# Performance work log

Hardware: AMD Instinct MI355X
Metric: run time of the kernel (lower is better)

## Reference

```python
import jax, jax.numpy as jnp
import numpy as np
from functools import partial

N_NODES = 50000
BN_EPS = 1e-5


def _renumber(src, dst, mask, n_nodes):
    # Faithful to extract_batch_edge_idx: kept edges are relabeled by the rank of
    # their node id among the sorted unique node ids APPEARING in kept edges.
    m = mask.astype(jnp.int32)
    appear = jnp.zeros(n_nodes, jnp.int32)
    appear = appear.at[src].max(m)
    appear = appear.at[dst].max(m)
    new_id = jnp.cumsum(appear) - 1  # rank of each appearing node id
    s = jnp.where(mask, new_id[src], 0)
    d = jnp.where(mask, new_id[dst], 0)
    return s, d


def _gcn_conv(x, W, b, src, dst, ew, n):
    # PyG GCNConv: linear, add self-loops, symmetric normalization, scatter-add.
    xw = x @ W                                   # [n, out]
    deg = jax.ops.segment_sum(ew, dst, num_segments=n) + 1.0  # +1 self loop
    dinv = jax.lax.rsqrt(deg)
    norm = dinv[src] * dinv[dst] * ew            # masked edges -> 0 weight
    agg = jax.ops.segment_sum(norm[:, None] * xw[src], dst, num_segments=n)
    agg = agg + (dinv * dinv)[:, None] * xw      # self-loop contribution
    return agg + b


def setup_inputs() -> dict:
    key = jax.random.key(0)
    ks = jax.random.split(key, 8)
    R, N, E, B = 3, N_NODES, 1000000, 2048
    inp, hid, out = 256, 512, 256
    features = jax.random.normal(ks[0], (R, N, inp), jnp.float32)
    W1 = jax.random.normal(ks[1], (inp, hid), jnp.float32) * (1.0 / np.sqrt(inp))
    b1 = jnp.zeros((hid,), jnp.float32)
    W2 = jax.random.normal(ks[2], (hid, out), jnp.float32) * (1.0 / np.sqrt(hid))
    b2 = jnp.zeros((out,), jnp.float32)
    gamma = jnp.ones((hid,), jnp.float32)
    beta = jnp.zeros((hid,), jnp.float32)
    edge_index = jax.random.randint(ks[3], (R, 2, E), 0, N, jnp.int64)
    # distinct, sorted batch node ids (torch code iterates node values)
    batch_nodes = jnp.sort(jax.random.permutation(ks[4], N)[:B]).astype(jnp.int64)
    return {"features": features, "W1": W1, "b1": b1, "W2": W2, "b2": b2,
            "gamma": gamma, "beta": beta, "edge_index": edge_index,
            "batch_nodes": batch_nodes}


def reference(features, W1, b1, W2, b2, gamma, beta, edge_index, batch_nodes):
    R, N, _ = features.shape
    B = batch_nodes.shape[0]
    in_batch = jnp.zeros(N, bool).at[batch_nodes].set(True)
    outs = []
    for r in range(R):  # small fixed relation count
        src, dst = edge_index[r, 0], edge_index[r, 1]
        mask = in_batch[src] & in_batch[dst]
        ew = mask.astype(features.dtype)
        s, d = _renumber(src, dst, mask, N)
        x = features[r, batch_nodes]             # [B, inp]
        h = _gcn_conv(x, W1, b1, s, d, ew, B)    # [B, hid]
        # BatchNorm1d (training mode: biased batch stats)
        mu = h.mean(axis=0)
        var = h.var(axis=0)
        h = (h - mu) * jax.lax.rsqrt(var + BN_EPS) * gamma + beta
        outs.append(_gcn_conv(h, W2, b2, s, d, ew, B))  # [B, out]
    stacked = jnp.stack(outs, axis=0)            # [R, B, out]
    return stacked.reshape(B, -1)                # row-major reshape, as torch
```

## Files before the change

### kernel.cpp

```cpp
#include <hip/hip_runtime.h>
#include <hip/hip_bf16.h>
#include <stdint.h>
#include <stddef.h>

#define RNUM   3
#define NNODES 50000
#define ENUM   1000000
#define BATCH  2048
#define INP    256
#define HID    512
#define OUTC   256
#define BN_EPS 1e-5f

typedef __bf16 bf16x8 __attribute__((ext_vector_type(8)));
typedef float  f32x4  __attribute__((ext_vector_type(4)));

__device__ inline unsigned short f2bf(float f) {
    union { float f; unsigned u; } c; c.f = f;
    unsigned u = c.u;
    return (unsigned short)((u + 0x7fffu + ((u >> 16) & 1u)) >> 16);
}

__device__ inline uint4 pack8(float4 a, float4 b) {
    uint4 r;
    r.x = (unsigned)f2bf(a.x) | ((unsigned)f2bf(a.y) << 16);
    r.y = (unsigned)f2bf(a.z) | ((unsigned)f2bf(a.w) << 16);
    r.z = (unsigned)f2bf(b.x) | ((unsigned)f2bf(b.y) << 16);
    r.w = (unsigned)f2bf(b.z) | ((unsigned)f2bf(b.w) << 16);
    return r;
}

__global__ __launch_bounds__(256) void k_wt(const float* __restrict__ W1,
                                            const float* __restrict__ W2,
                                            unsigned short* __restrict__ W1T,
                                            unsigned short* __restrict__ W2T) {
    __shared__ float T[32][33];
    int z = blockIdx.z;
    const float* W = z ? W2 : W1;
    unsigned short* WT = z ? W2T : W1T;
    int K = z ? HID : INP;
    int N = z ? OUTC : HID;
    int kt = blockIdx.y, nt = blockIdx.x;
    if (kt * 32 >= K || nt * 32 >= N) return;
    int tx = threadIdx.x & 31, ty = threadIdx.x >> 5;
#pragma unroll
    for (int j = 0; j < 4; ++j)
        T[ty + j * 8][tx] = W[(size_t)(kt * 32 + ty + j * 8) * N + nt * 32 + tx];
    __syncthreads();
#pragma unroll
    for (int j = 0; j < 4; ++j)
        WT[(size_t)(nt * 32 + ty + j * 8) * K + kt * 32 + tx] = f2bf(T[tx][ty + j * 8]);
}

__global__ void k_prep(const int* __restrict__ bn, int* __restrict__ inv,
                       int* __restrict__ appear, float* __restrict__ deg,
                       float* __restrict__ musum, float* __restrict__ sqsum,
                       int* __restrict__ kcount) {
    int i = blockIdx.x * blockDim.x + threadIdx.x;
    if (i < NNODES) {
        int lo = 0, hi = BATCH;
        while (lo < hi) { int mid = (lo + hi) >> 1; if (bn[mid] < i) lo = mid + 1; else hi = mid; }
        inv[i] = (lo < BATCH && bn[lo] == i) ? lo : -1;
    }
    if (i < RNUM * BATCH) { appear[i] = 0; deg[i] = 0.0f; }
    if (i < RNUM * HID)   { musum[i] = 0.0f; sqsum[i] = 0.0f; }
    if (i < RNUM)         kcount[i] = 0;
}

__global__ void k_mask(const int* __restrict__ edge_index, const int* __restrict__ inv,
                       int* __restrict__ appear, int2* __restrict__ edges,
                       int* __restrict__ kcount) {
    int z = blockIdx.z;
    const int* src = edge_index + (size_t)z * 2 * ENUM;
    const int* dst = src + ENUM;
    int2* ed = edges + (size_t)z * ENUM;
    int* app = appear + z * BATCH;
    int stride = gridDim.x * blockDim.x;
    for (int e4 = blockIdx.x * blockDim.x + threadIdx.x; e4 < ENUM / 4; e4 += stride) {
        int4 s4 = ((const int4*)src)[e4];
        int4 d4 = ((const int4*)dst)[e4];
        int ss[4] = {s4.x, s4.y, s4.z, s4.w};
        int dd[4] = {d4.x, d4.y, d4.z, d4.w};
#pragma unroll
        for (int i = 0; i < 4; ++i) {
            int ps = inv[ss[i]];
            int pd = inv[dd[i]];
            if (ps >= 0 && pd >= 0) {
                int idx = atomicAdd(kcount + z, 1);
                ed[idx] = make_int2(ps, pd);
                app[ps] = 1;
                app[pd] = 1;
            }
        }
    }
}

__global__ __launch_bounds__(1024) void k_scanDeg(const int* __restrict__ appear,
                                                  int2* __restrict__ edges,
                                                  const int* __restrict__ kcount,
                                                  float* __restrict__ deg) {
    __shared__ int buf[2][BATCH];
    __shared__ float degs[BATCH];
    int z = blockIdx.x;
    const int* ap = appear + z * BATCH;
    int2* ed = edges + (size_t)z * ENUM;
    float* dg = deg + z * BATCH;
    int t = threadIdx.x;
    buf[0][t] = ap[t];
    buf[0][t + 1024] = ap[t + 1024];
    degs[t] = 0.0f; degs[t + 1024] = 0.0f;
    __syncthreads();
    int cur = 0;
    for (int off = 1; off < BATCH; off <<= 1) {
        int nxt = cur ^ 1;
        int i1 = t, i2 = t + 1024;
        buf[nxt][i1] = buf[cur][i1] + (i1 >= off ? buf[cur][i1 - off] : 0);
        buf[nxt][i2] = buf[cur][i2] + (i2 >= off ? buf[cur][i2 - off] : 0);
        __syncthreads();
        cur = nxt;
    }
    int K = kcount[z];
    for (int e = t; e < K; e += 1024) {
        int2 E = ed[e];
        int s = buf[cur][E.x] - 1;
        int d = buf[cur][E.y] - 1;
        ed[e] = make_int2(s, d);
        atomicAdd(&degs[d], 1.0f);
    }
    __syncthreads();
    dg[t] = degs[t];
    dg[t + 1024] = degs[t + 1024];
}

__global__ __launch_bounds__(256) void k_gemm1(
    const float* __restrict__ features, const int* __restrict__ bn,
    const unsigned short* __restrict__ W1T, const float* __restrict__ b1,
    const float* __restrict__ deg, float* __restrict__ xw, float* __restrict__ hbase) {
    __shared__ __align__(16) unsigned short As[64][40];
    __shared__ __align__(16) unsigned short Bs[64][40];
    int z = blockIdx.z;
    const float* feat = features + (size_t)z * NNODES * INP;
    const float* dgz = deg + z * BATCH;
    float* xwz = xw + (size_t)z * BATCH * HID;
    float* hbz = hbase + (size_t)z * BATCH * HID;
    int m0 = blockIdx.y * 64, n0 = blockIdx.x * 64;
    int t = threadIdx.x;
    int ar = t >> 2, aq = t & 3;
    int grow = bn[m0 + ar];
    const float* aptr = feat + (size_t)grow * INP + aq * 8;
    const unsigned short* bptr = W1T + (size_t)(n0 + ar) * INP + aq * 8;

    int lane = t & 63, wave = t >> 6;
    int wm = (wave & 1) * 32, wn = (wave >> 1) * 32;
    int ml = lane & 15, quad = lane >> 4, q8 = quad * 8;

    f32x4 acc[2][2] = {};
    for (int k0 = 0; k0 < INP; k0 += 32) {
        float4 a0 = *(const float4*)(aptr + k0);
        float4 a1 = *(const float4*)(aptr + k0 + 4);
        uint4 bv = *(const uint4*)(bptr + k0);
        *(uint4*)&As[ar][aq * 8] = pack8(a0, a1);
        *(uint4*)&Bs[ar][aq * 8] = bv;
        __syncthreads();
        bf16x8 af[2], bfr[2];
#pragma unroll
        for (int mi = 0; mi < 2; ++mi) af[mi]  = *(const bf16x8*)&As[wm + mi * 16 + ml][q8];
#pragma unroll
        for (int ni = 0; ni < 2; ++ni) bfr[ni] = *(const bf16x8*)&Bs[wn + ni * 16 + ml][q8];
#pragma unroll
        for (int mi = 0; mi < 2; ++mi)
#pragma unroll
            for (int ni = 0; ni < 2; ++ni)
                acc[mi][ni] = __builtin_amdgcn_mfma_f32_16x16x32_bf16(af[mi], bfr[ni], acc[mi][ni], 0, 0, 0);
        __syncthreads();
    }
#pragma unroll
    for (int mi = 0; mi < 2; ++mi)
#pragma unroll
        for (int r = 0; r < 4; ++r) {
            int row = m0 + wm + mi * 16 + quad * 4 + r;
            float d2 = 1.0f / (dgz[row] + 1.0f);
#pragma unroll
            for (int ni = 0; ni < 2; ++ni) {
                int col = n0 + wn + ni * 16 + ml;
                float c = acc[mi][ni][r];
                xwz[(size_t)row * HID + col] = c;
                hbz[(size_t)row * HID + col] = d2 * c + b1[col];
            }
        }
}

__global__ __launch_bounds__(256) void k_gemm2(
    const float* __restrict__ hbase, const float* __restrict__ musum,
    const float* __restrict__ sqsum, const float* __restrict__ gamma,
    const float* __restrict__ beta, const unsigned short* __restrict__ W2T,
    const float* __restrict__ b2, const float* __restrict__ deg,
    float* __restrict__ yw, float* __restrict__ out) {
    __shared__ __align__(16) unsigned short As[64][40];
    __shared__ __align__(16) unsigned short Bs[64][40];
    __shared__ __align__(16) float gs[HID];
    __shared__ __align__(16) float ss_[HID];
    int z = blockIdx.z;
    const float* hz = hbase + (size_t)z * BATCH * HID;
    const float* dgz = deg + z * BATCH;
    float* ywz = yw + (size_t)z * BATCH * OUTC;
    float* oz = out + (size_t)z * BATCH * OUTC;
    int m0 = blockIdx.y * 64, n0 = blockIdx.x * 64;
    int t = threadIdx.x;

#pragma unroll
    for (int c = t; c < HID; c += 256) {
        float mu = musum[z * HID + c] * (1.0f / BATCH);
        float ex2 = sqsum[z * HID + c] * (1.0f / BATCH);
        float var = ex2 - mu * mu;
        float g = rsqrtf(var + BN_EPS) * gamma[c];
        gs[c] = g;
        ss_[c] = beta[c] - mu * g;
    }
    __syncthreads();

    int ar = t >> 2, aq = t & 3;
    const float* aptr = hz + (size_t)(m0 + ar) * HID + aq * 8;
    const unsigned short* bptr = W2T + (size_t)(n0 + ar) * HID + aq * 8;

    int lane = t & 63, wave = t >> 6;
    int wm = (wave & 1) * 32, wn = (wave >> 1) * 32;
    int ml = lane & 15, quad = lane >> 4, q8 = quad * 8;

    f32x4 acc[2][2] = {};
    for (int k0 = 0; k0 < HID; k0 += 32) {
        float4 h0 = *(const float4*)(aptr + k0);
        float4 h1 = *(const float4*)(aptr + k0 + 4);
        float4 g0 = *(const float4*)(gs + k0 + aq * 8);
        float4 g1 = *(const float4*)(gs + k0 + aq * 8 + 4);
        float4 s0 = *(const float4*)(ss_ + k0 + aq * 8);
        float4 s1 = *(const float4*)(ss_ + k0 + aq * 8 + 4);
        float4 a0 = make_float4(h0.x * g0.x + s0.x, h0.y * g0.y + s0.y,
                                h0.z * g0.z + s0.z, h0.w * g0.w + s0.w);
        float4 a1 = make_float4(h1.x * g1.x + s1.x, h1.y * g1.y + s1.y,
                                h1.z * g1.z + s1.z, h1.w * g1.w + s1.w);
        uint4 bv = *(const uint4*)(bptr + k0);
        *(uint4*)&As[ar][aq * 8] = pack8(a0, a1);
        *(uint4*)&Bs[ar][aq * 8] = bv;
        __syncthreads();
        bf16x8 af[2], bfr[2];
#pragma unroll
        for (int mi = 0; mi < 2; ++mi) af[mi]  = *(const bf16x8*)&As[wm + mi * 16 + ml][q8];
#pragma unroll
        for (int ni = 0; ni < 2; ++ni) bfr[ni] = *(const bf16x8*)&Bs[wn + ni * 16 + ml][q8];
#pragma unroll
        for (int mi = 0; mi < 2; ++mi)
#pragma unroll
            for (int ni = 0; ni < 2; ++ni)
                acc[mi][ni] = __builtin_amdgcn_mfma_f32_16x16x32_bf16(af[mi], bfr[ni], acc[mi][ni], 0, 0, 0);
        __syncthreads();
    }
#pragma unroll
    for (int mi = 0; mi < 2; ++mi)
#pragma unroll
        for (int r = 0; r < 4; ++r) {
            int row = m0 + wm + mi * 16 + quad * 4 + r;
            float d2 = 1.0f / (dgz[row] + 1.0f);
#pragma unroll
            for (int ni = 0; ni < 2; ++ni) {
                int col = n0 + wn + ni * 16 + ml;
                float c = acc[mi][ni][r];
                ywz[(size_t)row * OUTC + col] = c;
                oz[(size_t)row * OUTC + col] = d2 * c + b2[col];
            }
        }
}

__global__ void k_agg(const int2* __restrict__ edges, const int* __restrict__ kcount,
                      const float* __restrict__ deg, const float* __restrict__ src_mat,
                      float* __restrict__ dst_mat, int ncol) {
    int z = blockIdx.z;
    int K = kcount[z];
    const int2* ed = edges + (size_t)z * ENUM;
    const float* dgz = deg + z * BATCH;
    const float* sm = src_mat + (size_t)z * BATCH * ncol;
    float* dm = dst_mat + (size_t)z * BATCH * ncol;
    int nq = ncol >> 2;
    for (int e = blockIdx.x; e < K; e += gridDim.x) {
        int2 E = ed[e];
        float w = rsqrtf(dgz[E.x] + 1.0f) * rsqrtf(dgz[E.y] + 1.0f);
        const float4* srow = (const float4*)(sm + (size_t)E.x * ncol);
        float* drow = dm + (size_t)E.y * ncol;
        for (int q = threadIdx.x; q < nq; q += blockDim.x) {
            float4 v = srow[q];
            atomicAdd(&drow[q * 4 + 0], w * v.x);
            atomicAdd(&drow[q * 4 + 1], w * v.y);
            atomicAdd(&drow[q * 4 + 2], w * v.z);
            atomicAdd(&drow[q * 4 + 3], w * v.w);
        }
    }
}

__global__ __launch_bounds__(256) void k_bnstats(const float* __restrict__ hbase,
                                                 float* __restrict__ musum,
                                                 float* __restrict__ sqsum) {
    int z = blockIdx.z;
    const float* h = hbase + (size_t)z * BATCH * HID;
    int c0 = threadIdx.x;
    int r0 = blockIdx.x * 32;
    float s1a = 0, s2a = 0, s1b = 0, s2b = 0;
    for (int rr = 0; rr < 32; ++rr) {
        const float* row = h + (size_t)(r0 + rr) * HID;
        float va = row[c0];
        float vb = row[c0 + 256];
        s1a += va; s2a += va * va;
        s1b += vb; s2b += vb * vb;
    }
    atomicAdd(&musum[z * HID + c0], s1a);       atomicAdd(&sqsum[z * HID + c0], s2a);
    atomicAdd(&musum[z * HID + c0 + 256], s1b); atomicAdd(&sqsum[z * HID + c0 + 256], s2b);
}

extern "C" void kernel_launch(void* const* d_in, const int* in_sizes, int n_in,
                              void* d_out, int out_size, void* d_ws, size_t ws_size,
                              hipStream_t stream) {
    const float* features    = (const float*)d_in[0];
    const float* W1          = (const float*)d_in[1];
    const float* b1          = (const float*)d_in[2];
    const float* W2          = (const float*)d_in[3];
    const float* b2          = (const float*)d_in[4];
    const float* gamma       = (const float*)d_in[5];
    const float* beta        = (const float*)d_in[6];
    const int*   edge_index  = (const int*)d_in[7];
    const int*   batch_nodes = (const int*)d_in[8];
    float* out = (float*)d_out;

    char* p = (char*)d_ws;
    size_t cur = 0;
    auto alloc = [&](size_t bytes) {
        void* r = p + cur;
        cur = (cur + bytes + 255) & ~(size_t)255;
        return r;
    };
    int*   inv    = (int*)  alloc(NNODES * sizeof(int));
    int*   appear = (int*)  alloc(RNUM * BATCH * sizeof(int));
    int*   kcount = (int*)  alloc(RNUM * sizeof(int));
    float* deg    = (float*)alloc(RNUM * BATCH * sizeof(float));
    float* musum  = (float*)alloc(RNUM * HID * sizeof(float));
    float* sqsum  = (float*)alloc(RNUM * HID * sizeof(float));
    unsigned short* W1T = (unsigned short*)alloc((size_t)HID * INP * sizeof(unsigned short));
    unsigned short* W2T = (unsigned short*)alloc((size_t)OUTC * HID * sizeof(unsigned short));
    int2*  edges  = (int2*) alloc((size_t)RNUM * ENUM * sizeof(int2));
    float* xw     = (float*)alloc((size_t)RNUM * BATCH * HID * sizeof(float));
    float* hbase  = (float*)alloc((size_t)RNUM * BATCH * HID * sizeof(float));
    float* yw     = (float*)alloc((size_t)RNUM * BATCH * OUTC * sizeof(float));
    (void)ws_size; (void)in_sizes; (void)n_in; (void)out_size;

    k_wt<<<dim3(16, 16, 2), 256, 0, stream>>>(W1, W2, W1T, W2T);
    k_prep<<<(NNODES + 255) / 256, 256, 0, stream>>>(batch_nodes, inv, appear, deg,
                                                     musum, sqsum, kcount);
    k_mask<<<dim3(512, 1, RNUM), 256, 0, stream>>>(edge_index, inv, appear, edges, kcount);
    k_scanDeg<<<RNUM, 1024, 0, stream>>>(appear, edges, kcount, deg);

    k_gemm1<<<dim3(HID / 64, BATCH / 64, RNUM), 256, 0, stream>>>(
        features, batch_nodes, W1T, b1, deg, xw, hbase);
    k_agg<<<dim3(256, 1, RNUM), 256, 0, stream>>>(edges, kcount, deg, xw, hbase, HID);

    k_bnstats<<<dim3(64, 1, RNUM), 256, 0, stream>>>(hbase, musum, sqsum);

    k_gemm2<<<dim3(OUTC / 64, BATCH / 64, RNUM), 256, 0, stream>>>(
        hbase, musum, sqsum, gamma, beta, W2T, b2, deg, yw, out);
    k_agg<<<dim3(256, 1, RNUM), 256, 0, stream>>>(edges, kcount, deg, yw, out, OUTC);
}
```

Baseline: 365.6 us.

## Fuse all GCN stages into one cooperative persistent kernel with grid syncs

Replaces the eight separate kernel launches with a single cooperative kernel of 256 persistent blocks. Each phase (weight transpose, prep, masking, scan/degree, GEMM1, aggregation, BN stats, GEMM2, aggregation) is separated by grid.sync(). The scan in the rank phase now uses wave shuffles instead of a double-buffered LDS scan. This removes launch gaps between stages, but caps parallelism at 256 blocks: the edge-masking pass loses its earlier 1536-block grid, the scan/degree phase runs on only 3 blocks while the rest wait, and every phase boundary adds a grid-wide barrier.

```diff
diff --git a/kernel.cpp b/kernel.cpp
--- a/kernel.cpp
+++ b/kernel.cpp
@@ -1,7 +1,10 @@
 #include <hip/hip_runtime.h>
+#include <hip/hip_cooperative_groups.h>
 #include <hip/hip_bf16.h>
 #include <stdint.h>
 #include <stddef.h>
+
+namespace cg = cooperative_groups;
 
 #define RNUM   3
 #define NNODES 50000
@@ -11,6 +14,7 @@
 #define HID    512
 #define OUTC   256
 #define BN_EPS 1e-5f
+#define NBLK   256
 
 typedef __bf16 bf16x8 __attribute__((ext_vector_type(8)));
 typedef float  f32x4  __attribute__((ext_vector_type(4)));
@@ -30,289 +34,304 @@
     return r;
 }
 
-__global__ __launch_bounds__(256) void k_wt(const float* __restrict__ W1,
-                                            const float* __restrict__ W2,
-                                            unsigned short* __restrict__ W1T,
-                                            unsigned short* __restrict__ W2T) {
-    __shared__ float T[32][33];
-    int z = blockIdx.z;
-    const float* W = z ? W2 : W1;
-    unsigned short* WT = z ? W2T : W1T;
-    int K = z ? HID : INP;
-    int N = z ? OUTC : HID;
-    int kt = blockIdx.y, nt = blockIdx.x;
-    if (kt * 32 >= K || nt * 32 >= N) return;
-    int tx = threadIdx.x & 31, ty = threadIdx.x >> 5;
-#pragma unroll
-    for (int j = 0; j < 4; ++j)
-        T[ty + j * 8][tx] = W[(size_t)(kt * 32 + ty + j * 8) * N + nt * 32 + tx];
-    __syncthreads();
-#pragma unroll
-    for (int j = 0; j < 4; ++j)
-        WT[(size_t)(nt * 32 + ty + j * 8) * K + kt * 32 + tx] = f2bf(T[tx][ty + j * 8]);
-}
-
-__global__ void k_prep(const int* __restrict__ bn, int* __restrict__ inv,
-                       int* __restrict__ appear, float* __restrict__ deg,
-                       float* __restrict__ musum, float* __restrict__ sqsum,
-                       int* __restrict__ kcount) {
-    int i = blockIdx.x * blockDim.x + threadIdx.x;
-    if (i < NNODES) {
+#define SMEM_BYTES 16512
+
+__global__ __launch_bounds__(256) void k_mega(
+    const float* __restrict__ features, const float* __restrict__ W1,
+    const float* __restrict__ b1, const float* __restrict__ W2,
+    const float* __restrict__ b2, const float* __restrict__ gamma,
+    const float* __restrict__ beta, const int* __restrict__ edge_index,
+    const int* __restrict__ bn, float* __restrict__ out,
+    int* __restrict__ inv, int* __restrict__ appear, int* __restrict__ kcount,
+    float* __restrict__ deg, float* __restrict__ musum, float* __restrict__ sqsum,
+    unsigned short* __restrict__ W1T, unsigned short* __restrict__ W2T,
+    int2* __restrict__ edges, float* __restrict__ xw,
+    float* __restrict__ hbase, float* __restrict__ yw)
+{
+    cg::grid_group grid = cg::this_grid();
+    __shared__ __align__(16) char smem[SMEM_BYTES];
+    const int bid = blockIdx.x, tid = threadIdx.x;
+    const int gid = bid * 256 + tid;
+
+    {
+        float (*T)[33] = (float (*)[33])smem;
+        int z = bid >> 7, rem = bid & 127;
+        const float* W = z ? W2 : W1;
+        unsigned short* WT = z ? W2T : W1T;
+        int K = z ? HID : INP, N = z ? OUTC : HID;
+        int kt = z ? (rem >> 3) : (rem >> 4);
+        int nt = z ? (rem & 7) : (rem & 15);
+        int tx = tid & 31, ty = tid >> 5;
+#pragma unroll
+        for (int j = 0; j < 4; ++j)
+            T[ty + j * 8][tx] = W[(size_t)(kt * 32 + ty + j * 8) * N + nt * 32 + tx];
+        __syncthreads();
+#pragma unroll
+        for (int j = 0; j < 4; ++j)
+            WT[(size_t)(nt * 32 + ty + j * 8) * K + kt * 32 + tx] = f2bf(T[tx][ty + j * 8]);
+    }
+    if (gid < NNODES) {
         int lo = 0, hi = BATCH;
-        while (lo < hi) { int mid = (lo + hi) >> 1; if (bn[mid] < i) lo = mid + 1; else hi = mid; }
-        inv[i] = (lo < BATCH && bn[lo] == i) ? lo : -1;
-    }
-    if (i < RNUM * BATCH) { appear[i] = 0; deg[i] = 0.0f; }
-    if (i < RNUM * HID)   { musum[i] = 0.0f; sqsum[i] = 0.0f; }
-    if (i < RNUM)         kcount[i] = 0;
-}
-
-__global__ void k_mask(const int* __restrict__ edge_index, const int* __restrict__ inv,
-                       int* __restrict__ appear, int2* __restrict__ edges,
-                       int* __restrict__ kcount) {
-    int z = blockIdx.z;
-    const int* src = edge_index + (size_t)z * 2 * ENUM;
-    const int* dst = src + ENUM;
-    int2* ed = edges + (size_t)z * ENUM;
-    int* app = appear + z * BATCH;
-    int stride = gridDim.x * blockDim.x;
-    for (int e4 = blockIdx.x * blockDim.x + threadIdx.x; e4 < ENUM / 4; e4 += stride) {
-        int4 s4 = ((const int4*)src)[e4];
-        int4 d4 = ((const int4*)dst)[e4];
-        int ss[4] = {s4.x, s4.y, s4.z, s4.w};
-        int dd[4] = {d4.x, d4.y, d4.z, d4.w};
-#pragma unroll
-        for (int i = 0; i < 4; ++i) {
-            int ps = inv[ss[i]];
-            int pd = inv[dd[i]];
-            if (ps >= 0 && pd >= 0) {
-                int idx = atomicAdd(kcount + z, 1);
-                ed[idx] = make_int2(ps, pd);
-                app[ps] = 1;
-                app[pd] = 1;
+        while (lo < hi) { int mid = (lo + hi) >> 1; if (bn[mid] < gid) lo = mid + 1; else hi = mid; }
+        inv[gid] = (lo < BATCH && bn[lo] == gid) ? lo : -1;
+    }
+    if (gid < RNUM * BATCH) appear[gid] = 0;
+    if (gid < RNUM * HID)   { musum[gid] = 0.0f; sqsum[gid] = 0.0f; }
+    if (gid < RNUM)         kcount[gid] = 0;
+    __threadfence();
+    grid.sync();
+
+    for (int z = 0; z < RNUM; ++z) {
+        const int* src = edge_index + (size_t)z * 2 * ENUM;
+        const int* dst = src + ENUM;
+        int2* ed = edges + (size_t)z * ENUM;
+        int* app = appear + z * BATCH;
+        for (int e4 = gid; e4 < ENUM / 4; e4 += NBLK * 256) {
+            int4 s4 = ((const int4*)src)[e4];
+            int4 d4 = ((const int4*)dst)[e4];
+            int ss4[4] = {s4.x, s4.y, s4.z, s4.w};
+            int dd4[4] = {d4.x, d4.y, d4.z, d4.w};
+#pragma unroll
+            for (int i = 0; i < 4; ++i) {
+                int ps = inv[ss4[i]];
+                int pd = inv[dd4[i]];
+                if (ps >= 0 && pd >= 0) {
+                    int idx = atomicAdd(kcount + z, 1);
+                    ed[idx] = make_int2(ps, pd);
+                    app[ps] = 1;
+                    app[pd] = 1;
+                }
             }
         }
     }
-}
-
-__global__ __launch_bounds__(1024) void k_scanDeg(const int* __restrict__ appear,
-                                                  int2* __restrict__ edges,
-                                                  const int* __restrict__ kcount,
-                                                  float* __restrict__ deg) {
-    __shared__ int buf[2][BATCH];
-    __shared__ float degs[BATCH];
-    int z = blockIdx.x;
-    const int* ap = appear + z * BATCH;
-    int2* ed = edges + (size_t)z * ENUM;
-    float* dg = deg + z * BATCH;
-    int t = threadIdx.x;
-    buf[0][t] = ap[t];
-    buf[0][t + 1024] = ap[t + 1024];
-    degs[t] = 0.0f; degs[t + 1024] = 0.0f;
-    __syncthreads();
-    int cur = 0;
-    for (int off = 1; off < BATCH; off <<= 1) {
-        int nxt = cur ^ 1;
-        int i1 = t, i2 = t + 1024;
-        buf[nxt][i1] = buf[cur][i1] + (i1 >= off ? buf[cur][i1 - off] : 0);
-        buf[nxt][i2] = buf[cur][i2] + (i2 >= off ? buf[cur][i2 - off] : 0);
+    __threadfence();
+    grid.sync();
+
+    if (bid < RNUM) {
+        int* rnk = (int*)smem;
+        float* degs = (float*)(smem + 8192);
+        int* wsum = (int*)(smem + 16384);
+        int z = bid;
+        const int* ap = appear + z * BATCH;
+        int2* ed = edges + (size_t)z * ENUM;
+        float* dg = deg + z * BATCH;
+        int v[8], s = 0, base = tid * 8;
+#pragma unroll
+        for (int j = 0; j < 8; ++j) { v[j] = ap[base + j]; s += v[j]; }
+        int lane = tid & 63, w = tid >> 6;
+        int x = s;
+#pragma unroll
+        for (int off = 1; off < 64; off <<= 1) {
+            int y = __shfl_up(x, off, 64);
+            if (lane >= off) x += y;
+        }
+        if (lane == 63) wsum[w] = x;
+        degs[tid] = 0.0f; degs[tid + 256] = 0.0f; degs[tid + 512] = 0.0f; degs[tid + 768] = 0.0f;
+        degs[tid + 1024] = 0.0f; degs[tid + 1280] = 0.0f; degs[tid + 1536] = 0.0f; degs[tid + 1792] = 0.0f;
         __syncthreads();
-        cur = nxt;
-    }
-    int K = kcount[z];
-    for (int e = t; e < K; e += 1024) {
-        int2 E = ed[e];
-        int s = buf[cur][E.x] - 1;
-        int d = buf[cur][E.y] - 1;
-        ed[e] = make_int2(s, d);
-        atomicAdd(&degs[d], 1.0f);
-    }
-    __syncthreads();
-    dg[t] = degs[t];
-    dg[t + 1024] = degs[t + 1024];
-}
-
-__global__ __launch_bounds__(256) void k_gemm1(
-    const float* __restrict__ features, const int* __restrict__ bn,
-    const unsigned short* __restrict__ W1T, const float* __restrict__ b1,
-    const float* __restrict__ deg, float* __restrict__ xw, float* __restrict__ hbase) {
-    __shared__ __align__(16) unsigned short As[64][40];
-    __shared__ __align__(16) unsigned short Bs[64][40];
-    int z = blockIdx.z;
-    const float* feat = features + (size_t)z * NNODES * INP;
-    const float* dgz = deg + z * BATCH;
-    float* xwz = xw + (size_t)z * BATCH * HID;
-    float* hbz = hbase + (size_t)z * BATCH * HID;
-    int m0 = blockIdx.y * 64, n0 = blockIdx.x * 64;
-    int t = threadIdx.x;
-    int ar = t >> 2, aq = t & 3;
-    int grow = bn[m0 + ar];
-    const float* aptr = feat + (size_t)grow * INP + aq * 8;
-    const unsigned short* bptr = W1T + (size_t)(n0 + ar) * INP + aq * 8;
-
-    int lane = t & 63, wave = t >> 6;
-    int wm = (wave & 1) * 32, wn = (wave >> 1) * 32;
-    int ml = lane & 15, quad = lane >> 4, q8 = quad * 8;
-
-    f32x4 acc[2][2] = {};
-    for (int k0 = 0; k0 < INP; k0 += 32) {
-        float4 a0 = *(const float4*)(aptr + k0);
-        float4 a1 = *(const float4*)(aptr + k0 + 4);
-        uint4 bv = *(const uint4*)(bptr + k0);
-        *(uint4*)&As[ar][aq * 8] = pack8(a0, a1);
-        *(uint4*)&Bs[ar][aq * 8] = bv;
+        int woff = 0;
+#pragma unroll
+        for (int k = 0; k < 4; ++k) if (k < w) woff += wsum[k];
+        int run = woff + x - s;
+#pragma unroll
+        for (int j = 0; j < 8; ++j) { run += v[j]; rnk[base + j] = run - 1; }
         __syncthreads();
-        bf16x8 af[2], bfr[2];
-#pragma unroll
-        for (int mi = 0; mi < 2; ++mi) af[mi]  = *(const bf16x8*)&As[wm + mi * 16 + ml][q8];
-#pragma unroll
-        for (int ni = 0; ni < 2; ++ni) bfr[ni] = *(const bf16x8*)&Bs[wn + ni * 16 + ml][q8];
-#pragma unroll
-        for (int mi = 0; mi < 2; ++mi)
-#pragma unroll
-            for (int ni = 0; ni < 2; ++ni)
-                acc[mi][ni] = __builtin_amdgcn_mfma_f32_16x16x32_bf16(af[mi], bfr[ni], acc[mi][ni], 0, 0, 0);
+        int K = kcount[z];
+        for (int e = tid; e < K; e += 256) {
+            int2 E = ed[e];
+            int ss2 = rnk[E.x], dd2 = rnk[E.y];
+            ed[e] = make_int2(ss2, dd2);
+            atomicAdd(&degs[dd2], 1.0f);
+        }
         __syncthreads();
-    }
-#pragma unroll
-    for (int mi = 0; mi < 2; ++mi)
-#pragma unroll
-        for (int r = 0; r < 4; ++r) {
-            int row = m0 + wm + mi * 16 + quad * 4 + r;
-            float d2 = 1.0f / (dgz[row] + 1.0f);
-#pragma unroll
-            for (int ni = 0; ni < 2; ++ni) {
-                int col = n0 + wn + ni * 16 + ml;
-                float c = acc[mi][ni][r];
-                xwz[(size_t)row * HID + col] = c;
-                hbz[(size_t)row * HID + col] = d2 * c + b1[col];
+        for (int i = tid; i < BATCH; i += 256) dg[i] = degs[i];
+    }
+    __threadfence();
+    grid.sync();
+
+    {
+        unsigned short (*As)[40] = (unsigned short (*)[40])smem;
+        unsigned short (*Bs)[40] = (unsigned short (*)[40])(smem + 5120);
+        int lane = tid & 63, wave = tid >> 6;
+        int wm = (wave & 1) * 32, wn = (wave >> 1) * 32;
+        int ml = lane & 15, quad = lane >> 4, q8 = quad * 8;
+        int ar = tid >> 2, aq = tid & 3;
+        for (int tile = bid; tile < 768; tile += NBLK) {
+            int z = tile >> 8, rem = tile & 255;
+            int m0 = (rem >> 3) * 64, n0 = (rem & 7) * 64;
+            const float* feat = features + (size_t)z * NNODES * INP;
+            const float* dgz = deg + z * BATCH;
+            float* xwz = xw + (size_t)z * BATCH * HID;
+            float* hbz = hbase + (size_t)z * BATCH * HID;
+            int grow = bn[m0 + ar];
+            const float* aptr = feat + (size_t)grow * INP + aq * 8;
+            const unsigned short* bptr = W1T + (size_t)(n0 + ar) * INP + aq * 8;
+            f32x4 acc[2][2] = {};
+            for (int k0 = 0; k0 < INP; k0 += 32) {
+                float4 a0 = *(const float4*)(aptr + k0);
+                float4 a1 = *(const float4*)(aptr + k0 + 4);
+                uint4 bv = *(const uint4*)(bptr + k0);
+                *(uint4*)&As[ar][aq * 8] = pack8(a0, a1);
+                *(uint4*)&Bs[ar][aq * 8] = bv;
+                __syncthreads();
+                bf16x8 af[2], bfr[2];
+#pragma unroll
+                for (int mi = 0; mi < 2; ++mi) af[mi]  = *(const bf16x8*)&As[wm + mi * 16 + ml][q8];
+#pragma unroll
+                for (int ni = 0; ni < 2; ++ni) bfr[ni] = *(const bf16x8*)&Bs[wn + ni * 16 + ml][q8];
+#pragma unroll
+                for (int mi = 0; mi < 2; ++mi)
+#pragma unroll
+                    for (int ni = 0; ni < 2; ++ni)
+                        acc[mi][ni] = __builtin_amdgcn_mfma_f32_16x16x32_bf16(af[mi], bfr[ni], acc[mi][ni], 0, 0, 0);
+                __syncthreads();
             }
-        }
-}
-
-__global__ __launch_bounds__(256) void k_gemm2(
-    const float* __restrict__ hbase, const float* __restrict__ musum,
-    const float* __restrict__ sqsum, const float* __restrict__ gamma,
-    const float* __restrict__ beta, const unsigned short* __restrict__ W2T,
-    const float* __restrict__ b2, const float* __restrict__ deg,
-    float* __restrict__ yw, float* __restrict__ out) {
-    __shared__ __align__(16) unsigned short As[64][40];
-    __shared__ __align__(16) unsigned short Bs[64][40];
-    __shared__ __align__(16) float gs[HID];
-    __shared__ __align__(16) float ss_[HID];
-    int z = blockIdx.z;
-    const float* hz = hbase + (size_t)z * BATCH * HID;
-    const float* dgz = deg + z * BATCH;
-    float* ywz = yw + (size_t)z * BATCH * OUTC;
-    float* oz = out + (size_t)z * BATCH * OUTC;
-    int m0 = blockIdx.y * 64, n0 = blockIdx.x * 64;
-    int t = threadIdx.x;
-
-#pragma unroll
-    for (int c = t; c < HID; c += 256) {
-        float mu = musum[z * HID + c] * (1.0f / BATCH);
-        float ex2 = sqsum[z * HID + c] * (1.0f / BATCH);
-        float var = ex2 - mu * mu;
-        float g = rsqrtf(var + BN_EPS) * gamma[c];
-        gs[c] = g;
-        ss_[c] = beta[c] - mu * g;
-    }
-    __syncthreads();
-
-    int ar = t >> 2, aq = t & 3;
-    const float* aptr = hz + (size_t)(m0 + ar) * HID + aq * 8;
-    const unsigned short* bptr = W2T + (size_t)(n0 + ar) * HID + aq * 8;
-
-    int lane = t & 63, wave = t >> 6;
-    int wm = (wave & 1) * 32, wn = (wave >> 1) * 32;
-    int ml = lane & 15, quad = lane >> 4, q8 = quad * 8;
-
-    f32x4 acc[2][2] = {};
-    for (int k0 = 0; k0 < HID; k0 += 32) {
-        float4 h0 = *(const float4*)(aptr + k0);
-        float4 h1 = *(const float4*)(aptr + k0 + 4);
-        float4 g0 = *(const float4*)(gs + k0 + aq * 8);
-        float4 g1 = *(const float4*)(gs + k0 + aq * 8 + 4);
-        float4 s0 = *(const float4*)(ss_ + k0 + aq * 8);
-        float4 s1 = *(const float4*)(ss_ + k0 + aq * 8 + 4);
-        float4 a0 = make_float4(h0.x * g0.x + s0.x, h0.y * g0.y + s0.y,
-                                h0.z * g0.z + s0.z, h0.w * g0.w + s0.w);
-        float4 a1 = make_float4(h1.x * g1.x + s1.x, h1.y * g1.y + s1.y,
-                                h1.z * g1.z + s1.z, h1.w * g1.w + s1.w);
-        uint4 bv = *(const uint4*)(bptr + k0);
-        *(uint4*)&As[ar][aq * 8] = pack8(a0, a1);
-        *(uint4*)&Bs[ar][aq * 8] = bv;
-        __syncthreads();
-        bf16x8 af[2], bfr[2];
-#pragma unroll
-        for (int mi = 0; mi < 2; ++mi) af[mi]  = *(const bf16x8*)&As[wm + mi * 16 + ml][q8];
-#pragma unroll
-        for (int ni = 0; ni < 2; ++ni) bfr[ni] = *(const bf16x8*)&Bs[wn + ni * 16 + ml][q8];
-#pragma unroll
-        for (int mi = 0; mi < 2; ++mi)
-#pragma unroll
-            for (int ni = 0; ni < 2; ++ni)
-                acc[mi][ni] = __builtin_amdgcn_mfma_f32_16x16x32_bf16(af[mi], bfr[ni], acc[mi][ni], 0, 0, 0);
-        __syncthreads();
-    }
-#pragma unroll
-    for (int mi = 0; mi < 2; ++mi)
-#pragma unroll
-        for (int r = 0; r < 4; ++r) {
-            int row = m0 + wm + mi * 16 + quad * 4 + r;
-            float d2 = 1.0f / (dgz[row] + 1.0f);
-#pragma unroll
-            for (int ni = 0; ni < 2; ++ni) {
-                int col = n0 + wn + ni * 16 + ml;
-                float c = acc[mi][ni][r];
-                ywz[(size_t)row * OUTC + col] = c;
-                oz[(size_t)row * OUTC + col] = d2 * c + b2[col];
+#pragma unroll
+            for (int mi = 0; mi < 2; ++mi)
+#pragma unroll
+                for (int r = 0; r < 4; ++r) {
+                    int row = m0 + wm + mi * 16 + quad * 4 + r;
+                    float d2 = 1.0f / (dgz[row] + 1.0f);
+#pragma unroll
+                    for (int ni = 0; ni < 2; ++ni) {
+                        int col = n0 + wn + ni * 16 + ml;
+                        float c = acc[mi][ni][r];
+                        xwz[(size_t)row * HID + col] = c;
+                        hbz[(size_t)row * HID + col] = d2 * c + b1[col];
+                    }
+                }
+        }
+    }
+    __threadfence();
+    grid.sync();
+
+    for (int z = 0; z < RNUM; ++z) {
+        int K = kcount[z];
+        const int2* ed = edges + (size_t)z * ENUM;
+        const float* dgz = deg + z * BATCH;
+        const float* sm = xw + (size_t)z * BATCH * HID;
+        float* dm = hbase + (size_t)z * BATCH * HID;
+        for (int e = bid; e < K; e += NBLK) {
+            int2 E = ed[e];
+            float w = rsqrtf(dgz[E.x] + 1.0f) * rsqrtf(dgz[E.y] + 1.0f);
+            const float* srow = sm + (size_t)E.x * HID;
+            float* drow = dm + (size_t)E.y * HID;
+            for (int c = tid; c < HID; c += 256)
+                atomicAdd(&drow[c], w * srow[c]);
+        }
+    }
+    __threadfence();
+    grid.sync();
+
+    if (bid < 192) {
+        int z = bid >> 6;
+        int r0 = (bid & 63) * 32;
+        const float* h = hbase + (size_t)z * BATCH * HID;
+        int c0 = tid;
+        float s1a = 0, s2a = 0, s1b = 0, s2b = 0;
+        for (int rr = 0; rr < 32; ++rr) {
+            const float* row = h + (size_t)(r0 + rr) * HID;
+            float va = row[c0];
+            float vb = row[c0 + 256];
+            s1a += va; s2a += va * va;
+            s1b += vb; s2b += vb * vb;
+        }
+        atomicAdd(&musum[z * HID + c0], s1a);       atomicAdd(&sqsum[z * HID + c0], s2a);
+        atomicAdd(&musum[z * HID + c0 + 256], s1b); atomicAdd(&sqsum[z * HID + c0 + 256], s2b);
+    }
+    __threadfence();
+    grid.sync();
+
+    {
+        unsigned short (*As)[40] = (unsigned short (*)[40])smem;
+        unsigned short (*Bs)[40] = (unsigned short (*)[40])(smem + 5120);
+        float* gs = (float*)(smem + 10240);
+        float* ss_ = (float*)(smem + 12288);
+        int lane = tid & 63, wave = tid >> 6;
+        int wm = (wave & 1) * 32, wn = (wave >> 1) * 32;
+        int ml = lane & 15, quad = lane >> 4, q8 = quad * 8;
+        int ar = tid >> 2, aq = tid & 3;
+        for (int tile = bid; tile < 384; tile += NBLK) {
+            int z = tile >> 7, rem = tile & 127;
+            int m0 = (rem >> 2) * 64, n0 = (rem & 3) * 64;
+            const float* hz = hbase + (size_t)z * BATCH * HID;
+            const float* dgz = deg + z * BATCH;
+            float* ywz = yw + (size_t)z * BATCH * OUTC;
+            float* oz = out + (size_t)z * BATCH * OUTC;
+#pragma unroll
+            for (int c = tid; c < HID; c += 256) {
+                float mu = musum[z * HID + c] * (1.0f / BATCH);
+                float ex2 = sqsum[z * HID + c] * (1.0f / BATCH);
+                float var = ex2 - mu * mu;
+                float g = rsqrtf(var + BN_EPS) * gamma[c];
+                gs[c] = g;
+                ss_[c] = beta[c] - mu * g;
             }
-        }
-}
-
-__global__ void k_agg(const int2* __restrict__ edges, const int* __restrict__ kcount,
-                      const float* __restrict__ deg, const float* __restrict__ src_mat,
-                      float* __restrict__ dst_mat, int ncol) {
-    int z = blockIdx.z;
-    int K = kcount[z];
-    const int2* ed = edges + (size_t)z * ENUM;
-    const float* dgz = deg + z * BATCH;
-    const float* sm = src_mat + (size_t)z * BATCH * ncol;
-    float* dm = dst_mat + (size_t)z * BATCH * ncol;
-    int nq = ncol >> 2;
-    for (int e = blockIdx.x; e < K; e += gridDim.x) {
-        int2 E = ed[e];
-        float w = rsqrtf(dgz[E.x] + 1.0f) * rsqrtf(dgz[E.y] + 1.0f);
-        const float4* srow = (const float4*)(sm + (size_t)E.x * ncol);
-        float* drow = dm + (size_t)E.y * ncol;
-        for (int q = threadIdx.x; q < nq; q += blockDim.x) {
-            float4 v = srow[q];
-            atomicAdd(&drow[q * 4 + 0], w * v.x);
-            atomicAdd(&drow[q * 4 + 1], w * v.y);
-            atomicAdd(&drow[q * 4 + 2], w * v.z);
-            atomicAdd(&drow[q * 4 + 3], w * v.w);
-        }
-    }
-}
-
-__global__ __launch_bounds__(256) void k_bnstats(const float* __restrict__ hbase,
-                                                 float* __restrict__ musum,
-                                                 float* __restrict__ sqsum) {
-    int z = blockIdx.z;
-    const float* h = hbase + (size_t)z * BATCH * HID;
-    int c0 = threadIdx.x;
-    int r0 = blockIdx.x * 32;
-    float s1a = 0, s2a = 0, s1b = 0, s2b = 0;
-    for (int rr = 0; rr < 32; ++rr) {
-        const float* row = h + (size_t)(r0 + rr) * HID;
-        float va = row[c0];
-        float vb = row[c0 + 256];
-        s1a += va; s2a += va * va;
-        s1b += vb; s2b += vb * vb;
-    }
-    atomicAdd(&musum[z * HID + c0], s1a);       atomicAdd(&sqsum[z * HID + c0], s2a);
-    atomicAdd(&musum[z * HID + c0 + 256], s1b); atomicAdd(&sqsum[z * HID + c0 + 256], s2b);
+            __syncthreads();
+            const float* aptr = hz + (size_t)(m0 + ar) * HID + aq * 8;
+            const unsigned short* bptr = W2T + (size_t)(n0 + ar) * HID + aq * 8;
+            f32x4 acc[2][2] = {};
+            for (int k0 = 0; k0 < HID; k0 += 32) {
+                float4 h0 = *(const float4*)(aptr + k0);
+                float4 h1 = *(const float4*)(aptr + k0 + 4);
+                float4 g0 = *(const float4*)(gs + k0 + aq * 8);
+                float4 g1 = *(const float4*)(gs + k0 + aq * 8 + 4);
+                float4 s0 = *(const float4*)(ss_ + k0 + aq * 8);
+                float4 s1 = *(const float4*)(ss_ + k0 + aq * 8 + 4);
+                float4 a0 = make_float4(h0.x * g0.x + s0.x, h0.y * g0.y + s0.y,
+                                        h0.z * g0.z + s0.z, h0.w * g0.w + s0.w);
+                float4 a1 = make_float4(h1.x * g1.x + s1.x, h1.y * g1.y + s1.y,
+                                        h1.z * g1.z + s1.z, h1.w * g1.w + s1.w);
+                uint4 bv = *(const uint4*)(bptr + k0);
+                *(uint4*)&As[ar][aq * 8] = pack8(a0, a1);
+                *(uint4*)&Bs[ar][aq * 8] = bv;
+                __syncthreads();
+                bf16x8 af[2], bfr[2];
+#pragma unroll
+                for (int mi = 0; mi < 2; ++mi) af[mi]  = *(const bf16x8*)&As[wm + mi * 16 + ml][q8];
+#pragma unroll
+                for (int ni = 0; ni < 2; ++ni) bfr[ni] = *(const bf16x8*)&Bs[wn + ni * 16 + ml][q8];
+#pragma unroll
+                for (int mi = 0; mi < 2; ++mi)
+#pragma unroll
+                    for (int ni = 0; ni < 2; ++ni)
+                        acc[mi][ni] = __builtin_amdgcn_mfma_f32_16x16x32_bf16(af[mi], bfr[ni], acc[mi][ni], 0, 0, 0);
+                __syncthreads();
+            }
+#pragma unroll
+            for (int mi = 0; mi < 2; ++mi)
+#pragma unroll
+                for (int r = 0; r < 4; ++r) {
+                    int row = m0 + wm + mi * 16 + quad * 4 + r;
+                    float d2 = 1.0f / (dgz[row] + 1.0f);
+#pragma unroll
+                    for (int ni = 0; ni < 2; ++ni) {
+                        int col = n0 + wn + ni * 16 + ml;
+                        float c = acc[mi][ni][r];
+                        ywz[(size_t)row * OUTC + col] = c;
+                        oz[(size_t)row * OUTC + col] = d2 * c + b2[col];
+                    }
+                }
+        }
+    }
+    __threadfence();
+    grid.sync();
+
+    for (int z = 0; z < RNUM; ++z) {
+        int K = kcount[z];
+        const int2* ed = edges + (size_t)z * ENUM;
+        const float* dgz = deg + z * BATCH;
+        const float* sm = yw + (size_t)z * BATCH * OUTC;
+        float* dm = out + (size_t)z * BATCH * OUTC;
+        for (int e = bid; e < K; e += NBLK) {
+            int2 E = ed[e];
+            float w = rsqrtf(dgz[E.x] + 1.0f) * rsqrtf(dgz[E.y] + 1.0f);
+            const float* srow = sm + (size_t)E.x * OUTC;
+            float* drow = dm + (size_t)E.y * OUTC;
+            for (int c = tid; c < OUTC; c += 256)
+                atomicAdd(&drow[c], w * srow[c]);
+        }
+    }
 }
 
 extern "C" void kernel_launch(void* const* d_in, const int* in_sizes, int n_in,
@@ -350,19 +369,13 @@
     float* yw     = (float*)alloc((size_t)RNUM * BATCH * OUTC * sizeof(float));
     (void)ws_size; (void)in_sizes; (void)n_in; (void)out_size;
 
-    k_wt<<<dim3(16, 16, 2), 256, 0, stream>>>(W1, W2, W1T, W2T);
-    k_prep<<<(NNODES + 255) / 256, 256, 0, stream>>>(batch_nodes, inv, appear, deg,
-                                                     musum, sqsum, kcount);
-    k_mask<<<dim3(512, 1, RNUM), 256, 0, stream>>>(edge_index, inv, appear, edges, kcount);
-    k_scanDeg<<<RNUM, 1024, 0, stream>>>(appear, edges, kcount, deg);
-
-    k_gemm1<<<dim3(HID / 64, BATCH / 64, RNUM), 256, 0, stream>>>(
-        features, batch_nodes, W1T, b1, deg, xw, hbase);
-    k_agg<<<dim3(256, 1, RNUM), 256, 0, stream>>>(edges, kcount, deg, xw, hbase, HID);
-
-    k_bnstats<<<dim3(64, 1, RNUM), 256, 0, stream>>>(hbase, musum, sqsum);
-
-    k_gemm2<<<dim3(OUTC / 64, BATCH / 64, RNUM), 256, 0, stream>>>(
-        hbase, musum, sqsum, gamma, beta, W2T, b2, deg, yw, out);
-    k_agg<<<dim3(256, 1, RNUM), 256, 0, stream>>>(edges, kcount, deg, yw, out, OUTC);
+    void* args[] = {
+        (void*)&features, (void*)&W1, (void*)&b1, (void*)&W2, (void*)&b2,
+        (void*)&gamma, (void*)&beta, (void*)&edge_index, (void*)&batch_nodes,
+        (void*)&out, (void*)&inv, (void*)&appear, (void*)&kcount, (void*)&deg,
+        (void*)&musum, (void*)&sqsum, (void*)&W1T, (void*)&W2T, (void*)&edges,
+        (void*)&xw, (void*)&hbase, (void*)&yw
+    };
+    hipLaunchCooperativeKernel((const void*)k_mega, dim3(NBLK), dim3(256),
+                               args, 0, stream);
 }
```

Result: slower. 725.9 us (+98.5%).
